# Kernel optimization log

Hardware: AMD Instinct MI355X
Metric: run time of the kernel (lower is better)

The kernel has to match this reference:

```python
import jax, jax.numpy as jnp
import numpy as np

B, T, D, H = 4, 2048, 1024, 16
Dh = D // H          # 64 head dim
NF = Dh // 2         # 32 rotary frequencies


def setup_inputs() -> dict:
    key = jax.random.key(0)
    k0, k1, k2, k3 = jax.random.split(key, 4)
    x = jax.random.normal(k0, (B, T, D), dtype=jnp.float32)
    # 3D spatial coordinates per token, e.g. voxel positions
    coords = jax.random.uniform(k1, (B, T, 3), dtype=jnp.float32, minval=0.0, maxval=64.0)
    w_scale = 1.0 / np.sqrt(D)
    qkv_w = jax.random.normal(k2, (3 * D, D), dtype=jnp.float32) * w_scale
    qkv_b = jnp.zeros((3 * D,), dtype=jnp.float32)
    proj_w = jax.random.normal(k3, (D, D), dtype=jnp.float32) * w_scale
    proj_b = jnp.zeros((D,), dtype=jnp.float32)
    # mixed-axis rope: frequency f uses coordinate axis (f % 3), geometric period spacing within each axis group
    axes = (jnp.arange(NF) % 3).astype(jnp.int32)
    group = (jnp.arange(NF) // 3).astype(jnp.float32)
    n_per_axis = float(NF) / 3.0
    inv_freq = (10000.0 ** (-group / n_per_axis)).astype(jnp.float32)
    return {"x": x, "coords": coords, "qkv_w": qkv_w, "qkv_b": qkv_b,
            "proj_w": proj_w, "proj_b": proj_b, "inv_freq": inv_freq, "axes": axes}


def _apply_rope(t, sin, cos):
    # t: [B, H, T, Dh]; sin/cos: [B, 1, T, Dh//2]  (rotate-half convention)
    t1, t2 = jnp.split(t, 2, axis=-1)
    return jnp.concatenate([t1 * cos - t2 * sin, t1 * sin + t2 * cos], axis=-1)


def reference(x, coords, qkv_w, qkv_b, proj_w, proj_b, inv_freq, axes):
    b, t, d = x.shape
    # fused QKV projection
    qkv = (x @ qkv_w.T + qkv_b).reshape(b, t, 3, H, Dh)
    qkv = jnp.transpose(qkv, (2, 0, 3, 1, 4))     # [3, B, H, T, Dh]
    q, k, v = qkv[0], qkv[1], qkv[2]
    # vectorized per-sample rope from coords (replaces python loop over batch)
    ang = jnp.take(coords, axes, axis=-1) * inv_freq      # [B, T, NF]
    sin = jnp.sin(ang)[:, None]                            # [B, 1, T, NF]
    cos = jnp.cos(ang)[:, None]
    q = _apply_rope(q, sin, cos)
    k = _apply_rope(k, sin, cos)
    # standard scaling mode: single 1/sqrt(Dh) inside SDPA
    scale = 1.0 / np.sqrt(Dh)
    scores = jnp.einsum('bhqd,bhkd->bhqk', q, k) * scale
    attn = jax.nn.softmax(scores, axis=-1)
    out = jnp.einsum('bhqk,bhkd->bhqd', attn, v)           # [B, H, T, Dh]
    out = jnp.transpose(out, (0, 2, 1, 3)).reshape(b, t, d)
    return out @ proj_w.T + proj_b
```

## Files before the change

### kernel.cpp

```cpp
#include <hip/hip_runtime.h>
#include <hip/hip_bf16.h>

#define B_ 4
#define T_ 2048
#define D_ 1024
#define H_ 16
#define DH 64
#define NF 32
#define BH (B_*H_)
#define M_ROWS (B_*T_)

#define QSCALE 0.125f

using u16 = unsigned short;
using u32 = unsigned int;

typedef __bf16 bf16x8 __attribute__((ext_vector_type(8)));
typedef float  f32x4  __attribute__((ext_vector_type(4)));

__device__ __forceinline__ u16 f2bf(float f) {
  u32 u = __float_as_uint(f);
  u32 r = u + 0x7fffu + ((u >> 16) & 1u);
  return (u16)(r >> 16);
}
__device__ __forceinline__ u16 f2bf_hw(float f) {
  __bf16 h = (__bf16)f;
  return *(u16*)&h;
}
__device__ __forceinline__ float bf2f(u16 h) {
  return __uint_as_float(((u32)h) << 16);
}

__device__ __forceinline__ void gload_lds16(const void* g, void* l) {
  __builtin_amdgcn_global_load_lds((__attribute__((address_space(1))) void*)(g),
                                   (__attribute__((address_space(3))) void*)(l),
                                   16, 0, 0);
}

__global__ __launch_bounds__(256)
void cvt_kernel(const float* __restrict__ in, u16* __restrict__ out, int n8) {
  int idx = blockIdx.x * 256 + threadIdx.x;
  if (idx >= n8) return;
  const float4* p = (const float4*)in + (long)idx * 2;
  float4 a = p[0], b = p[1];
  u32 o0 = (u32)f2bf(a.x) | ((u32)f2bf(a.y) << 16);
  u32 o1 = (u32)f2bf(a.z) | ((u32)f2bf(a.w) << 16);
  u32 o2 = (u32)f2bf(b.x) | ((u32)f2bf(b.y) << 16);
  u32 o3 = (u32)f2bf(b.z) | ((u32)f2bf(b.w) << 16);
  ((uint4*)out)[idx] = make_uint4(o0, o1, o2, o3);
}

__global__ __launch_bounds__(256)
void sincos_kernel(const float* __restrict__ coords, const float* __restrict__ inv_freq,
                   const int* __restrict__ axes, float* __restrict__ sc) {
  int idx = blockIdx.x * 256 + threadIdx.x;
  if (idx >= B_ * T_ * NF) return;
  int f = idx & 31;
  long bt = idx >> 5;
  float c = coords[bt * 3 + axes[f]];
  float ang = c * inv_freq[f];
  sc[bt * 64 + f]      = sinf(ang);
  sc[bt * 64 + 32 + f] = cosf(ang);
}

__global__ __launch_bounds__(256, 2)
void gemm_qkv(const u16* __restrict__ A, const u16* __restrict__ Bt,
              const float* __restrict__ bias, const float* __restrict__ sc,
              u16* __restrict__ qr, u16* __restrict__ kr, u16* __restrict__ vbuf) {
  const int N = 3 * D_, K = D_;
  __shared__ u16 As[128 * 64];
  __shared__ u16 Bs[128 * 64];
  int nb = N >> 7;
  int bid = blockIdx.x;
  int nwg = gridDim.x;
  int cpx = nwg >> 3;
  bid = (bid & 7) * cpx + (bid >> 3);
  int bm = bid / nb, bn = bid % nb;
  long m0 = (long)bm << 7, n0 = (long)bn << 7;
  int tid = threadIdx.x;
  int lane = tid & 63, w = tid >> 6;
  int g = lane >> 4, lr = lane & 15;
  int wm = w >> 1, wn = w & 1;

  f32x4 acc[4][4] = {};

  for (int kt = 0; kt < K; kt += 64) {
    __syncthreads();
    #pragma unroll
    for (int j = 0; j < 4; ++j) {
      int ob = j * 4096 + tid * 16;
      int row = ob >> 7, col = (ob & 127) >> 1;
      u16* ldsA = As + j * 2048 + w * 512;
      u16* ldsB = Bs + j * 2048 + w * 512;
      gload_lds16(A + (m0 + row) * K + kt + col, ldsA);
      gload_lds16(Bt + (n0 + row) * K + kt + col, ldsB);
    }
    __syncthreads();
    #pragma unroll
    for (int kk = 0; kk < 2; ++kk) {
      bf16x8 af[4], bfr[4];
      #pragma unroll
      for (int i = 0; i < 4; ++i)
        af[i] = *(const bf16x8*)(As + (wm * 64 + i * 16 + lr) * 64 + kk * 32 + g * 8);
      #pragma unroll
      for (int i = 0; i < 4; ++i)
        bfr[i] = *(const bf16x8*)(Bs + (wn * 64 + i * 16 + lr) * 64 + kk * 32 + g * 8);
      #pragma unroll
      for (int mi = 0; mi < 4; ++mi)
        #pragma unroll
        for (int nj = 0; nj < 4; ++nj)
          acc[mi][nj] = __builtin_amdgcn_mfma_f32_16x16x32_bf16(af[mi], bfr[nj], acc[mi][nj], 0, 0, 0);
    }
  }

  int part = (int)(n0 >> 10);
  int h = ((int)(n0 & 1023) >> 6) + wn;
  float bv[4];
  #pragma unroll
  for (int nj = 0; nj < 4; ++nj)
    bv[nj] = bias[n0 + wn * 64 + nj * 16 + lr];

  #pragma unroll
  for (int mi = 0; mi < 4; ++mi) {
    #pragma unroll
    for (int i = 0; i < 4; ++i) {
      long row = m0 + wm * 64 + mi * 16 + g * 4 + i;
      int b = (int)(row >> 11), t = (int)(row & 2047);
      long obase = ((long)(b * 16 + h) * T_ + t) * 64;
      if (part == 2) {
        #pragma unroll
        for (int nj = 0; nj < 4; ++nj)
          vbuf[obase + nj * 16 + lr] = f2bf(acc[mi][nj][i] + bv[nj]);
      } else {
        u16* outp = part ? kr : qr;
        float fac = part ? 1.0f : QSCALE;
        const float* scp = sc + row * 64;
        #pragma unroll
        for (int nj = 0; nj < 2; ++nj) {
          int d = nj * 16 + lr;
          float sn = scp[d], cs = scp[32 + d];
          float t1 = acc[mi][nj][i]     + bv[nj];
          float t2 = acc[mi][nj + 2][i] + bv[nj + 2];
          outp[obase + d]      = f2bf((t1 * cs - t2 * sn) * fac);
          outp[obase + 32 + d] = f2bf((t1 * sn + t2 * cs) * fac);
        }
      }
    }
  }
}

__global__ __launch_bounds__(256, 2)
void gemm_bt(const u16* __restrict__ A, const u16* __restrict__ Bt,
             const float* __restrict__ bias, float* __restrict__ Cout,
             int M, int N, int K) {
  __shared__ u16 As[128 * 64];
  __shared__ u16 Bs[128 * 64];
  int nb = N >> 7;
  int bid = blockIdx.x;
  int nwg = gridDim.x;
  if ((nwg & 7) == 0) {
    int c = nwg >> 3;
    bid = (bid & 7) * c + (bid >> 3);
  }
  int bm = bid / nb, bn = bid % nb;
  long m0 = (long)bm << 7, n0 = (long)bn << 7;
  int tid = threadIdx.x;
  int lane = tid & 63, w = tid >> 6;
  int g = lane >> 4, lr = lane & 15;
  int wm = w >> 1, wn = w & 1;

  f32x4 acc[4][4] = {};

  for (int kt = 0; kt < K; kt += 64) {
    __syncthreads();
    #pragma unroll
    for (int j = 0; j < 4; ++j) {
      int ob = j * 4096 + tid * 16;
      int row = ob >> 7, col = (ob & 127) >> 1;
      u16* ldsA = As + j * 2048 + w * 512;
      u16* ldsB = Bs + j * 2048 + w * 512;
      gload_lds16(A + (m0 + row) * K + kt + col, ldsA);
      gload_lds16(Bt + (n0 + row) * K + kt + col, ldsB);
    }
    __syncthreads();
    #pragma unroll
    for (int kk = 0; kk < 2; ++kk) {
      bf16x8 af[4], bfr[4];
      #pragma unroll
      for (int i = 0; i < 4; ++i)
        af[i] = *(const bf16x8*)(As + (wm * 64 + i * 16 + lr) * 64 + kk * 32 + g * 8);
      #pragma unroll
      for (int i = 0; i < 4; ++i)
        bfr[i] = *(const bf16x8*)(Bs + (wn * 64 + i * 16 + lr) * 64 + kk * 32 + g * 8);
      #pragma unroll
      for (int mi = 0; mi < 4; ++mi)
        #pragma unroll
        for (int nj = 0; nj < 4; ++nj)
          acc[mi][nj] = __builtin_amdgcn_mfma_f32_16x16x32_bf16(af[mi], bfr[nj], acc[mi][nj], 0, 0, 0);
    }
  }
  #pragma unroll
  for (int mi = 0; mi < 4; ++mi) {
    #pragma unroll
    for (int nj = 0; nj < 4; ++nj) {
      long col = n0 + wn * 64 + nj * 16 + lr;
      float bvv = bias[col];
      #pragma unroll
      for (int i = 0; i < 4; ++i) {
        long row = m0 + wm * 64 + mi * 16 + g * 4 + i;
        Cout[row * (long)N + col] = acc[mi][nj][i] + bvv;
      }
    }
  }
}

__global__ __launch_bounds__(256)
void vtrans_kernel(const u16* __restrict__ vbuf, u16* __restrict__ vt) {
  __shared__ u16 Vsm[128 * 72];
  int bh = blockIdx.y;
  int t0 = blockIdx.x << 7;
  int tid = threadIdx.x;
  #pragma unroll
  for (int it = 0; it < 4; ++it) {
    int item = it * 256 + tid;
    int tl = item >> 3, dg = item & 7;
    uint4 u = *(const uint4*)(vbuf + ((long)bh * T_ + t0 + tl) * 64 + dg * 8);
    *(uint4*)(Vsm + tl * 72 + dg * 8) = u;
  }
  __syncthreads();
  int d = tid >> 2, tc = tid & 3;
  long obase = ((long)bh * DH + d) * T_ + t0 + tc * 32;
  #pragma unroll
  for (int c = 0; c < 4; ++c) {
    u32 o[4];
    #pragma unroll
    for (int j = 0; j < 4; ++j) {
      u16 lo = Vsm[(tc * 32 + c * 8 + 2 * j)     * 72 + d];
      u16 hi = Vsm[(tc * 32 + c * 8 + 2 * j + 1) * 72 + d];
      o[j] = (u32)lo | ((u32)hi << 16);
    }
    *(uint4*)(vt + obase + c * 8) = make_uint4(o[0], o[1], o[2], o[3]);
  }
}

__global__ __launch_bounds__(256, 3)
void attn_kernel(const u16* __restrict__ Qr, const u16* __restrict__ Kr,
                 const u16* __restrict__ Vt, u16* __restrict__ Aout) {
  __shared__ u16 Ks[2][64 * 64];
  __shared__ u16 Vs[2][64 * 64];
  __shared__ u16 Ps[4][32 * 64];
  int wg = (blockIdx.x & 7) * 128 + (blockIdx.x >> 3);
  int bh = wg >> 4;
  int b = bh >> 4, h = bh & 15;
  int q0 = (wg & 15) << 7;
  int tid = threadIdx.x;
  int lane = tid & 63, w = tid >> 6;
  int g = lane >> 4, lr = lane & 15;

  const long tbase = (long)bh * T_;
  const long vbase = (long)bh * DH;

  bf16x8 aq[2][2];
  #pragma unroll
  for (int mi = 0; mi < 2; ++mi)
    #pragma unroll
    for (int kk = 0; kk < 2; ++kk)
      aq[mi][kk] = *(const bf16x8*)(Qr + (tbase + q0 + w * 32 + mi * 16 + lr) * DH + kk * 32 + g * 8);

  f32x4 oacc[2][4] = {};
  float lsum[2][4] = {};

  const int swz0 = ((0 + g) ^ (lr & 7)) << 3;
  const int swz1 = ((4 + g) ^ (lr & 7)) << 3;

  auto STAGE = [&](int buf, int kb) {
    #pragma unroll
    for (int j = 0; j < 2; ++j) {
      int ob = j * 4096 + tid * 16;
      int row = ob >> 7;
      int c = ((ob >> 4) & 7) ^ (row & 7);
      u16* ldsK = Ks[buf] + j * 2048 + w * 512;
      u16* ldsV = Vs[buf] + j * 2048 + w * 512;
      gload_lds16(Kr + (tbase + kb + row) * DH + c * 8, ldsK);
      gload_lds16(Vt + (vbase + row) * T_ + kb + c * 8, ldsV);
    }
  };

  STAGE(0, 0);
  asm volatile("s_waitcnt vmcnt(0)" ::: "memory");
  __builtin_amdgcn_s_barrier();
  __builtin_amdgcn_sched_barrier(0);

  int cur = 0;
  for (int kt = 0; kt < T_ / 64; ++kt) {
    if (kt + 1 < T_ / 64) STAGE(cur ^ 1, (kt + 1) * 64);

    const u16* kbuf = Ks[cur];
    const u16* vbuf = Vs[cur];

    f32x4 s[2][4] = {};
    #pragma unroll
    for (int kk = 0; kk < 2; ++kk) {
      int so = kk ? swz1 : swz0;
      bf16x8 bk[4];
      #pragma unroll
      for (int nj = 0; nj < 4; ++nj)
        bk[nj] = *(const bf16x8*)(kbuf + (nj * 16 + lr) * 64 + so);
      #pragma unroll
      for (int mi = 0; mi < 2; ++mi)
        #pragma unroll
        for (int nj = 0; nj < 4; ++nj)
          s[mi][nj] = __builtin_amdgcn_mfma_f32_16x16x32_bf16(aq[mi][kk], bk[nj], s[mi][nj], 0, 0, 0);
    }

    u16* pw = Ps[w];
    #pragma unroll
    for (int mi = 0; mi < 2; ++mi) {
      #pragma unroll
      for (int i = 0; i < 4; ++i) {
        float p0 = __expf(s[mi][0][i]);
        float p1 = __expf(s[mi][1][i]);
        float p2 = __expf(s[mi][2][i]);
        float p3 = __expf(s[mi][3][i]);
        lsum[mi][i] += (p0 + p1) + (p2 + p3);
        int rowp = mi * 16 + g * 4 + i;
        int kx = (rowp & 7) << 3;
        int rb = rowp * 64;
        pw[rb + ((lr)      ^ kx)] = f2bf_hw(p0);
        pw[rb + ((lr + 16) ^ kx)] = f2bf_hw(p1);
        pw[rb + ((lr + 32) ^ kx)] = f2bf_hw(p2);
        pw[rb + ((lr + 48) ^ kx)] = f2bf_hw(p3);
      }
    }
    asm volatile("s_waitcnt lgkmcnt(0)" ::: "memory");
    __builtin_amdgcn_sched_barrier(0);

    #pragma unroll
    for (int kk = 0; kk < 2; ++kk) {
      int so = kk ? swz1 : swz0;
      bf16x8 ap[2], bv[4];
      #pragma unroll
      for (int mi = 0; mi < 2; ++mi)
        ap[mi] = *(const bf16x8*)(pw + (mi * 16 + lr) * 64 + so);
      #pragma unroll
      for (int nj = 0; nj < 4; ++nj)
        bv[nj] = *(const bf16x8*)(vbuf + (nj * 16 + lr) * 64 + so);
      #pragma unroll
      for (int mi = 0; mi < 2; ++mi)
        #pragma unroll
        for (int nj = 0; nj < 4; ++nj)
          oacc[mi][nj] = __builtin_amdgcn_mfma_f32_16x16x32_bf16(ap[mi], bv[nj], oacc[mi][nj], 0, 0, 0);
    }

    __builtin_amdgcn_sched_barrier(0);
    asm volatile("s_waitcnt vmcnt(0)" ::: "memory");
    __builtin_amdgcn_s_barrier();
    __builtin_amdgcn_sched_barrier(0);
    cur ^= 1;
  }

  #pragma unroll
  for (int mi = 0; mi < 2; ++mi) {
    #pragma unroll
    for (int i = 0; i < 4; ++i) {
      float l = lsum[mi][i];
      #pragma unroll
      for (int dd = 1; dd < 16; dd <<= 1) l += __shfl_xor(l, dd);
      float inv = 1.0f / l;
      long q = q0 + w * 32 + mi * 16 + g * 4 + i;
      long obase = ((long)b * T_ + q) * D_ + h * DH;
      #pragma unroll
      for (int nj = 0; nj < 4; ++nj)
        Aout[obase + nj * 16 + lr] = f2bf_hw(oacc[mi][nj][i] * inv);
    }
  }
}

extern "C" void kernel_launch(void* const* d_in, const int* in_sizes, int n_in,
                              void* d_out, int out_size, void* d_ws, size_t ws_size,
                              hipStream_t stream) {
  const float* x        = (const float*)d_in[0];
  const float* coords   = (const float*)d_in[1];
  const float* qkv_w    = (const float*)d_in[2];
  const float* qkv_b    = (const float*)d_in[3];
  const float* proj_w   = (const float*)d_in[4];
  const float* proj_b   = (const float*)d_in[5];
  const float* inv_freq = (const float*)d_in[6];
  const int*   axes     = (const int*)d_in[7];
  float* out = (float*)d_out;

  char* ws = (char*)d_ws;
  size_t off = 0;
  auto alloc = [&](size_t bytes) -> char* {
    char* p = ws + off;
    off += (bytes + 255) & ~(size_t)255;
    return p;
  };
  u16*   xb     = (u16*)  alloc((size_t)M_ROWS * D_ * 2);
  u16*   wqkv   = (u16*)  alloc((size_t)3 * D_ * D_ * 2);
  u16*   wproj  = (u16*)  alloc((size_t)D_ * D_ * 2);
  float* sc     = (float*)alloc((size_t)M_ROWS * 64 * 4);
  u16*   qr     = (u16*)  alloc((size_t)BH * T_ * DH * 2);
  u16*   kr     = (u16*)  alloc((size_t)BH * T_ * DH * 2);
  u16*   vbuf   = (u16*)  alloc((size_t)BH * T_ * DH * 2);
  u16*   vt     = (u16*)  alloc((size_t)BH * T_ * DH * 2);
  u16*   aout   = vbuf;

  cvt_kernel<<<(M_ROWS * D_ / 8 + 255) / 256, 256, 0, stream>>>(x, xb, M_ROWS * D_ / 8);
  cvt_kernel<<<(3 * D_ * D_ / 8 + 255) / 256, 256, 0, stream>>>(qkv_w, wqkv, 3 * D_ * D_ / 8);
  cvt_kernel<<<(D_ * D_ / 8 + 255) / 256, 256, 0, stream>>>(proj_w, wproj, D_ * D_ / 8);
  sincos_kernel<<<(B_ * T_ * NF + 255) / 256, 256, 0, stream>>>(coords, inv_freq, axes, sc);

  gemm_qkv<<<(M_ROWS / 128) * (3 * D_ / 128), 256, 0, stream>>>(xb, wqkv, qkv_b, sc,
                                                                qr, kr, vbuf);
  vtrans_kernel<<<dim3(T_ / 128, BH), 256, 0, stream>>>(vbuf, vt);
  attn_kernel<<<1024, 256, 0, stream>>>(qr, kr, vt, aout);
  gemm_bt<<<(M_ROWS / 128) * (D_ / 128), 256, 0, stream>>>(aout, wproj, proj_b, out,
                                                           M_ROWS, D_, D_);
}
```

Baseline: 226.8 us.

## Switch attention to transposed 32x32 MFMA with register-resident P via permlane swap

Rewrites the attention inner loop to compute S^T with 32x32x16 MFMAs using K as the A operand and Q as B. The exponentiated probabilities are then repacked in registers through permlane32_swap and fed directly as the B operand of the PV MFMA. This removes the per-wave LDS round trip for P and its lgkmcnt wait, and frees LDS so occupancy is raised to 4 blocks. The risk is higher register pressure from the 16-wide accumulators, plus layout subtleties in the swap that correctness depends on.

```diff
diff --git a/kernel.cpp b/kernel.cpp
--- a/kernel.cpp
+++ b/kernel.cpp
@@ -17,6 +17,8 @@
 
 typedef __bf16 bf16x8 __attribute__((ext_vector_type(8)));
 typedef float  f32x4  __attribute__((ext_vector_type(4)));
+typedef float  f32x16 __attribute__((ext_vector_type(16)));
+typedef unsigned uint2v __attribute__((ext_vector_type(2)));
 
 __device__ __forceinline__ u16 f2bf(float f) {
   u32 u = __float_as_uint(f);
@@ -27,8 +29,23 @@
   __bf16 h = (__bf16)f;
   return *(u16*)&h;
 }
+__device__ __forceinline__ u32 pack2(float lo, float hi) {
+  return (u32)f2bf_hw(lo) | ((u32)f2bf_hw(hi) << 16);
+}
 __device__ __forceinline__ float bf2f(u16 h) {
   return __uint_as_float(((u32)h) << 16);
+}
+
+__device__ __forceinline__ void pl32swap(u32 a, u32 b, int hb, u32& x, u32& y) {
+#if __has_builtin(__builtin_amdgcn_permlane32_swap)
+  uint2v r = __builtin_amdgcn_permlane32_swap(a, b, false, false);
+  x = r.x; y = r.y;
+#else
+  u32 xa = (u32)__shfl_xor((int)a, 32);
+  u32 xb = (u32)__shfl_xor((int)b, 32);
+  x = hb ? xb : a;
+  y = hb ? b : xa;
+#endif
 }
 
 __device__ __forceinline__ void gload_lds16(const void* g, void* l) {
@@ -243,35 +260,31 @@
   }
 }
 
-__global__ __launch_bounds__(256, 3)
+__global__ __launch_bounds__(256, 4)
 void attn_kernel(const u16* __restrict__ Qr, const u16* __restrict__ Kr,
                  const u16* __restrict__ Vt, u16* __restrict__ Aout) {
   __shared__ u16 Ks[2][64 * 64];
   __shared__ u16 Vs[2][64 * 64];
-  __shared__ u16 Ps[4][32 * 64];
   int wg = (blockIdx.x & 7) * 128 + (blockIdx.x >> 3);
   int bh = wg >> 4;
   int b = bh >> 4, h = bh & 15;
   int q0 = (wg & 15) << 7;
   int tid = threadIdx.x;
   int lane = tid & 63, w = tid >> 6;
-  int g = lane >> 4, lr = lane & 15;
+  int l5 = lane & 31, hb = lane >> 5;
 
   const long tbase = (long)bh * T_;
   const long vbase = (long)bh * DH;
 
-  bf16x8 aq[2][2];
-  #pragma unroll
-  for (int mi = 0; mi < 2; ++mi)
-    #pragma unroll
-    for (int kk = 0; kk < 2; ++kk)
-      aq[mi][kk] = *(const bf16x8*)(Qr + (tbase + q0 + w * 32 + mi * 16 + lr) * DH + kk * 32 + g * 8);
-
-  f32x4 oacc[2][4] = {};
-  float lsum[2][4] = {};
-
-  const int swz0 = ((0 + g) ^ (lr & 7)) << 3;
-  const int swz1 = ((4 + g) ^ (lr & 7)) << 3;
+  bf16x8 bq[4];
+  #pragma unroll
+  for (int s = 0; s < 4; ++s)
+    bq[s] = *(const bf16x8*)(Qr + (tbase + q0 + w * 32 + l5) * DH + s * 16 + hb * 8);
+
+  f32x16 oacc0 = {}, oacc1 = {};
+  float lsum = 0.f;
+
+  const int sl = l5 & 7;
 
   auto STAGE = [&](int buf, int kb) {
     #pragma unroll
@@ -298,58 +311,47 @@
     const u16* kbuf = Ks[cur];
     const u16* vbuf = Vs[cur];
 
-    f32x4 s[2][4] = {};
-    #pragma unroll
-    for (int kk = 0; kk < 2; ++kk) {
-      int so = kk ? swz1 : swz0;
-      bf16x8 bk[4];
-      #pragma unroll
-      for (int nj = 0; nj < 4; ++nj)
-        bk[nj] = *(const bf16x8*)(kbuf + (nj * 16 + lr) * 64 + so);
-      #pragma unroll
-      for (int mi = 0; mi < 2; ++mi)
-        #pragma unroll
-        for (int nj = 0; nj < 4; ++nj)
-          s[mi][nj] = __builtin_amdgcn_mfma_f32_16x16x32_bf16(aq[mi][kk], bk[nj], s[mi][nj], 0, 0, 0);
-    }
-
-    u16* pw = Ps[w];
-    #pragma unroll
-    for (int mi = 0; mi < 2; ++mi) {
-      #pragma unroll
-      for (int i = 0; i < 4; ++i) {
-        float p0 = __expf(s[mi][0][i]);
-        float p1 = __expf(s[mi][1][i]);
-        float p2 = __expf(s[mi][2][i]);
-        float p3 = __expf(s[mi][3][i]);
-        lsum[mi][i] += (p0 + p1) + (p2 + p3);
-        int rowp = mi * 16 + g * 4 + i;
-        int kx = (rowp & 7) << 3;
-        int rb = rowp * 64;
-        pw[rb + ((lr)      ^ kx)] = f2bf_hw(p0);
-        pw[rb + ((lr + 16) ^ kx)] = f2bf_hw(p1);
-        pw[rb + ((lr + 32) ^ kx)] = f2bf_hw(p2);
-        pw[rb + ((lr + 48) ^ kx)] = f2bf_hw(p3);
-      }
-    }
-    asm volatile("s_waitcnt lgkmcnt(0)" ::: "memory");
-    __builtin_amdgcn_sched_barrier(0);
-
-    #pragma unroll
-    for (int kk = 0; kk < 2; ++kk) {
-      int so = kk ? swz1 : swz0;
-      bf16x8 ap[2], bv[4];
-      #pragma unroll
-      for (int mi = 0; mi < 2; ++mi)
-        ap[mi] = *(const bf16x8*)(pw + (mi * 16 + lr) * 64 + so);
-      #pragma unroll
-      for (int nj = 0; nj < 4; ++nj)
-        bv[nj] = *(const bf16x8*)(vbuf + (nj * 16 + lr) * 64 + so);
-      #pragma unroll
-      for (int mi = 0; mi < 2; ++mi)
-        #pragma unroll
-        for (int nj = 0; nj < 4; ++nj)
-          oacc[mi][nj] = __builtin_amdgcn_mfma_f32_16x16x32_bf16(ap[mi], bv[nj], oacc[mi][nj], 0, 0, 0);
+    f32x16 p0 = {}, p1 = {};
+    #pragma unroll
+    for (int s = 0; s < 4; ++s) {
+      int c = ((2 * s + hb) ^ sl) * 8;
+      bf16x8 ak0 = *(const bf16x8*)(kbuf + l5 * 64 + c);
+      bf16x8 ak1 = *(const bf16x8*)(kbuf + (32 + l5) * 64 + c);
+      p0 = __builtin_amdgcn_mfma_f32_32x32x16_bf16(ak0, bq[s], p0, 0, 0, 0);
+      p1 = __builtin_amdgcn_mfma_f32_32x32x16_bf16(ak1, bq[s], p1, 0, 0, 0);
+    }
+
+    u32 pA[8], pB[8];
+    #pragma unroll
+    for (int r4 = 0; r4 < 4; ++r4) {
+      float a0 = __expf(p0[4 * r4 + 0]);
+      float a1 = __expf(p0[4 * r4 + 1]);
+      float a2 = __expf(p0[4 * r4 + 2]);
+      float a3 = __expf(p0[4 * r4 + 3]);
+      lsum += (a0 + a1) + (a2 + a3);
+      pA[r4] = pack2(a0, a1);
+      pB[r4] = pack2(a2, a3);
+      float b0 = __expf(p1[4 * r4 + 0]);
+      float b1 = __expf(p1[4 * r4 + 1]);
+      float b2 = __expf(p1[4 * r4 + 2]);
+      float b3 = __expf(p1[4 * r4 + 3]);
+      lsum += (b0 + b1) + (b2 + b3);
+      pA[4 + r4] = pack2(b0, b1);
+      pB[4 + r4] = pack2(b2, b3);
+    }
+
+    #pragma unroll
+    for (int s2 = 0; s2 < 4; ++s2) {
+      u32 w0, w2, w1, w3;
+      pl32swap(pA[2 * s2], pA[2 * s2 + 1], hb, w0, w2);
+      pl32swap(pB[2 * s2], pB[2 * s2 + 1], hb, w1, w3);
+      union { u32 u[4]; bf16x8 v; } bw;
+      bw.u[0] = w0; bw.u[1] = w1; bw.u[2] = w2; bw.u[3] = w3;
+      int c = ((2 * s2 + hb) ^ sl) * 8;
+      bf16x8 av0 = *(const bf16x8*)(vbuf + l5 * 64 + c);
+      bf16x8 av1 = *(const bf16x8*)(vbuf + (32 + l5) * 64 + c);
+      oacc0 = __builtin_amdgcn_mfma_f32_32x32x16_bf16(av0, bw.v, oacc0, 0, 0, 0);
+      oacc1 = __builtin_amdgcn_mfma_f32_32x32x16_bf16(av1, bw.v, oacc1, 0, 0, 0);
     }
 
     __builtin_amdgcn_sched_barrier(0);
@@ -359,20 +361,18 @@
     cur ^= 1;
   }
 
-  #pragma unroll
-  for (int mi = 0; mi < 2; ++mi) {
-    #pragma unroll
-    for (int i = 0; i < 4; ++i) {
-      float l = lsum[mi][i];
-      #pragma unroll
-      for (int dd = 1; dd < 16; dd <<= 1) l += __shfl_xor(l, dd);
-      float inv = 1.0f / l;
-      long q = q0 + w * 32 + mi * 16 + g * 4 + i;
-      long obase = ((long)b * T_ + q) * D_ + h * DH;
-      #pragma unroll
-      for (int nj = 0; nj < 4; ++nj)
-        Aout[obase + nj * 16 + lr] = f2bf_hw(oacc[mi][nj][i] * inv);
-    }
+  lsum += __shfl_xor(lsum, 32);
+  float inv = 1.0f / lsum;
+  long row = (long)b * T_ + q0 + w * 32 + l5;
+  u16* ob = Aout + row * D_ + h * DH;
+  #pragma unroll
+  for (int r4 = 0; r4 < 4; ++r4) {
+    u32 w0 = pack2(oacc0[4 * r4 + 0] * inv, oacc0[4 * r4 + 1] * inv);
+    u32 w1 = pack2(oacc0[4 * r4 + 2] * inv, oacc0[4 * r4 + 3] * inv);
+    *(uint2*)(ob + r4 * 8 + hb * 4) = make_uint2(w0, w1);
+    u32 w2 = pack2(oacc1[4 * r4 + 0] * inv, oacc1[4 * r4 + 1] * inv);
+    u32 w3 = pack2(oacc1[4 * r4 + 2] * inv, oacc1[4 * r4 + 3] * inv);
+    *(uint2*)(ob + 32 + r4 * 8 + hb * 4) = make_uint2(w2, w3);
   }
 }
 
```

Result: no change. 224.0 us (-1.2%).
